# Performance work log

Hardware: AMD Instinct MI355X
Metric: run time of the kernel (lower is better)

## Reference

```python
import jax, jax.numpy as jnp
import numpy as np

N_NODES = 50000
N_EDGES = 1_600_000
N_REL = 8
D_IN = 128
D_OUT = 128


def _unique_edges(rng, n_nodes, n_rel, n_edges):
    # Torch module clamps the dense adjacency to 0/1, so duplicate
    # (rel, src, dst) triples collapse; generate unique edges so the
    # edge-list formulation matches exactly.
    m = 2 * n_edges
    src = rng.integers(0, n_nodes, m)
    dst = rng.integers(0, n_nodes, m)
    et = rng.integers(0, n_rel, m)
    key = (et.astype(np.int64) * n_nodes + src) * n_nodes + dst
    _, idx = np.unique(key, return_index=True)
    idx = np.sort(idx)[:n_edges]
    return src[idx], dst[idx], et[idx]


def setup_inputs() -> dict:
    key = jax.random.key(0)
    kx, kw, kr, kb = jax.random.split(key, 4)
    rng = np.random.default_rng(0)
    src, dst, et = _unique_edges(rng, N_NODES, N_REL, N_EDGES)
    bound = 1.0 / np.sqrt(D_OUT)
    return {
        "x": jax.random.normal(kx, (N_NODES, D_IN), dtype=jnp.float32),
        "edge_index": jnp.asarray(np.stack([src, dst]), dtype=jnp.int64),
        "edge_type": jnp.asarray(et, dtype=jnp.int64),
        "weight": jax.random.uniform(kw, (N_REL, D_OUT, D_IN), minval=-bound, maxval=bound, dtype=jnp.float32),
        "root": jax.random.uniform(kr, (D_OUT, D_IN), minval=-bound, maxval=bound, dtype=jnp.float32),
        "bias": jax.random.uniform(kb, (D_OUT,), minval=-bound, maxval=bound, dtype=jnp.float32),
    }


def reference(x, edge_index, edge_type, weight, root, bias):
    # Math identical to: adj[l, src, dst] = 1; adj row-normalized (mean);
    # out = sum_r norm_adj_r @ x @ W_r^T + x @ root^T + bias.
    n_rel, d_out, d_in = weight.shape
    n_nodes = x.shape[0]
    src = edge_index[0]
    dst = edge_index[1]
    seg = (edge_type * n_nodes + src).astype(jnp.int32)  # segment per (rel, node)
    num_seg = n_rel * n_nodes
    # sum of neighbor features per (relation, node): [R*N, d_in]
    agg = jax.ops.segment_sum(x[dst], seg, num_segments=num_seg)
    deg = jax.ops.segment_sum(jnp.ones((src.shape[0],), dtype=x.dtype), seg, num_segments=num_seg)
    norm = jnp.where(deg > 0, 1.0 / deg, 0.0)[:, None]  # mean aggr, nan_to_num(0)
    agg = (agg * norm).reshape(n_rel, n_nodes, d_in)
    out = jnp.einsum('rnd,rod->no', agg, weight)
    out = out + x @ root.T + bias[None]
    return out
```

## Files before the change

kernel.cpp:

```cpp
#include <hip/hip_runtime.h>


#define D 128
#define SCAN_CHUNK 2048
#define SEG_BITS 9
#define SEGS_PER_BUCKET 512
#define NBLK 128
#define NDEG 32

typedef __attribute__((ext_vector_type(8))) short short8;
typedef __attribute__((ext_vector_type(4))) float v4f;
typedef __attribute__((ext_vector_type(2))) float f32x2;
typedef __attribute__((ext_vector_type(4))) unsigned uint4v;

#define GLOAD_LDS16(gptr, lptr) \
    __builtin_amdgcn_global_load_lds((const __attribute__((address_space(1))) void*)(gptr), \
                                     (__attribute__((address_space(3))) void*)(lptr), 16, 0, 0)

__device__ __forceinline__ unsigned short f2b(float f) {
    union { float f; unsigned u; } v; v.f = f;
    unsigned r = v.u + 0x7fffu + ((v.u >> 16) & 1u);
    return (unsigned short)(r >> 16);
}
__device__ __forceinline__ float blo(unsigned u) {
    union { unsigned u; float f; } v; v.u = u << 16; return v.f;
}
__device__ __forceinline__ float bhi(unsigned u) {
    union { unsigned u; float f; } v; v.u = u & 0xffff0000u; return v.f;
}

__global__ void cvt_bf16_all(const float* __restrict__ x, long long nx,
                             const float* __restrict__ w, long long nw,
                             const float* __restrict__ root, long long nr,
                             unsigned short* __restrict__ xB,
                             unsigned short* __restrict__ xRow,
                             unsigned short* __restrict__ wB, int nN) {
    long long i = ((long long)blockIdx.x * blockDim.x + threadIdx.x) * 4;
    if (i < nx) {
        float4 v = *(const float4*)(x + i);
        uint2 p;
        p.x = (unsigned)f2b(v.x) | ((unsigned)f2b(v.y) << 16);
        p.y = (unsigned)f2b(v.z) | ((unsigned)f2b(v.w) << 16);
        long long n = i >> 7;
        int d = (int)(i & 127);
        size_t o = (size_t)(d >> 5) * (size_t)nN * 32 + (size_t)n * 32 + (d & 31);
        *(uint2*)(xB + o) = p;
        *(uint2*)(xRow + i) = p;
        return;
    }
    const float* src;
    unsigned short* dst;
    long long j;
    if (i < nx + nw) { src = w; dst = wB; j = i - nx; }
    else if (i < nx + nw + nr) { src = root; dst = wB + nw; j = i - nx - nw; }
    else return;
    float4 v = *(const float4*)(src + j);
    uint2 p;
    p.x = (unsigned)f2b(v.x) | ((unsigned)f2b(v.y) << 16);
    p.y = (unsigned)f2b(v.z) | ((unsigned)f2b(v.w) << 16);
    *(uint2*)(dst + j) = p;
}

__global__ __launch_bounds__(256)
void histA(const int* __restrict__ ei, const int* __restrict__ et,
           int* __restrict__ blockHist, int nE, int nN, int B, int epb) {
    __shared__ int lh[1024];
    const int tid = threadIdx.x;
    for (int b = tid; b < B; b += 256) lh[b] = 0;
    __syncthreads();
    const int base = blockIdx.x * epb;
    const int lim = min(base + epb, nE);
    for (int e = base + tid; e < lim; e += 256) {
        int seg = et[e] * nN + ei[e];
        atomicAdd(&lh[seg >> SEG_BITS], 1);
    }
    __syncthreads();
    for (int b = tid; b < B; b += 256)
        blockHist[b * NBLK + blockIdx.x] = lh[b];
}

__global__ __launch_bounds__(256)
void scan1(const int* __restrict__ in, int* __restrict__ excl,
           int* __restrict__ blockSums, int n) {
    __shared__ int t[256];
    const int tid = threadIdx.x;
    const int base = blockIdx.x * SCAN_CHUNK + tid * 8;
    int v[8];
    int tot = 0;
#pragma unroll
    for (int i = 0; i < 8; i++) {
        v[i] = (base + i < n) ? in[base + i] : 0;
        tot += v[i];
    }
    t[tid] = tot;
    __syncthreads();
    for (int off = 1; off < 256; off <<= 1) {
        int add = (tid >= off) ? t[tid - off] : 0;
        __syncthreads();
        t[tid] += add;
        __syncthreads();
    }
    int run = t[tid] - tot;
#pragma unroll
    for (int i = 0; i < 8; i++) {
        if (base + i < n) excl[base + i] = run;
        run += v[i];
    }
    if (tid == 255) blockSums[blockIdx.x] = t[255];
}

__global__ __launch_bounds__(256)
void scan2(int* __restrict__ blockSums, int nb) {
    __shared__ int t[256];
    const int tid = threadIdx.x;
    int v = (tid < nb) ? blockSums[tid] : 0;
    t[tid] = v;
    __syncthreads();
    for (int off = 1; off < 256; off <<= 1) {
        int add = (tid >= off) ? t[tid - off] : 0;
        __syncthreads();
        t[tid] += add;
        __syncthreads();
    }
    if (tid < nb) blockSums[tid] = t[tid] - v;
}

__global__ __launch_bounds__(256)
void scatterA(const int* __restrict__ ei, const int* __restrict__ et,
              const int* __restrict__ scanned, const int* __restrict__ blockSums,
              unsigned* __restrict__ bucketEdges,
              int nE, int nN, int B, int epb) {
    __shared__ int cur[1024];
    const int tid = threadIdx.x;
    for (int b = tid; b < B; b += 256) {
        int idx = b * NBLK + blockIdx.x;
        cur[b] = scanned[idx] + blockSums[idx >> 11];
    }
    __syncthreads();
    const int base = blockIdx.x * epb;
    const int lim = min(base + epb, nE);
    for (int e = base + tid; e < lim; e += 256) {
        int seg = et[e] * nN + ei[e];
        int bkt = seg >> SEG_BITS;
        unsigned pk = ((unsigned)(seg & (SEGS_PER_BUCKET - 1)) << 16) | (unsigned)ei[nE + e];
        int pos = atomicAdd(&cur[bkt], 1);
        bucketEdges[pos] = pk;
    }
}

__global__ __launch_bounds__(256)
void segOff(const unsigned* __restrict__ bucketEdges, const int* __restrict__ scanned,
            const int* __restrict__ blockSums,
            int* __restrict__ off, unsigned short* __restrict__ sortedDst,
            int* __restrict__ perm, int nE, int numSeg, int B) {
    __shared__ int lh[SEGS_PER_BUCKET];
    __shared__ int sc[256];
    __shared__ int lcur[SEGS_PER_BUCKET];
    __shared__ int dcnt[256];
    __shared__ int dbase[256];
    const int tid = threadIdx.x;
    const int b = blockIdx.x;
    const int i0 = b * NBLK;
    const int eBase = scanned[i0] + blockSums[i0 >> 11];
    int eEnd = nE;
    if (b + 1 < B) {
        const int i1 = (b + 1) * NBLK;
        eEnd = scanned[i1] + blockSums[i1 >> 11];
    }
    const int segBase = b * SEGS_PER_BUCKET;
    const int segLim = min(SEGS_PER_BUCKET, numSeg - segBase);

    lh[2 * tid] = 0; lh[2 * tid + 1] = 0;
    dcnt[tid] = 0;
    __syncthreads();
    for (int i = eBase + tid; i < eEnd; i += 256)
        atomicAdd(&lh[bucketEdges[i] >> 16], 1);
    __syncthreads();
    const int li0 = 2 * tid, li1 = 2 * tid + 1;
    const int sub = li0 >> 6;
    int a0 = lh[li0], a1 = lh[li1];
    int b0 = min(a0, NDEG - 1), b1 = min(a1, NDEG - 1), r0 = 0, r1 = 0;
    if (li0 < segLim) r0 = atomicAdd(&dcnt[sub * NDEG + b0], 1);
    if (li1 < segLim) r1 = atomicAdd(&dcnt[sub * NDEG + b1], 1);
    sc[tid] = a0 + a1;
    __syncthreads();
    for (int o = 1; o < 256; o <<= 1) {
        int add = (tid >= o) ? sc[tid - o] : 0;
        __syncthreads();
        sc[tid] += add;
        __syncthreads();
    }
    int pairBase = sc[tid] - (a0 + a1);
    int g0 = eBase + pairBase;
    int g1 = g0 + a0;
    lcur[li0] = g0;
    lcur[li1] = g1;
    if (li0 < segLim) off[segBase + li0] = g0;
    if (li1 < segLim) off[segBase + li1] = g1;
    if (b == B - 1 && tid == 0) off[numSeg] = nE;
    if (tid < 8) {
        int run = 0;
#pragma unroll
        for (int k = 0; k < NDEG; k++) { dbase[tid * NDEG + k] = run; run += dcnt[tid * NDEG + k]; }
    }
    __syncthreads();
    if (li0 < segLim) perm[segBase + sub * 64 + dbase[sub * NDEG + b0] + r0] = segBase + li0;
    if (li1 < segLim) perm[segBase + sub * 64 + dbase[sub * NDEG + b1] + r1] = segBase + li1;
    for (int i = eBase + tid; i < eEnd; i += 256) {
        unsigned u = bucketEdges[i];
        int pos = atomicAdd(&lcur[u >> 16], 1);
        sortedDst[pos] = (unsigned short)(u & 0xFFFFu);
    }
}

__global__ __launch_bounds__(256)
void rgcn_gather(const unsigned short* __restrict__ xB,
                 const unsigned short* __restrict__ sortedDst,
                 const int* __restrict__ off, const int* __restrict__ perm,
                 unsigned short* __restrict__ Abuf, int nN, int numSeg,
                 size_t SL, unsigned long long M) {
    const int tid = threadIdx.x;
    const int lane = tid & 63;
    const int idx4 = lane & 3;
    const int grp = lane >> 2;
    const int wv = tid >> 6;
    const int gsi = blockIdx.x * 64 + wv * 16 + grp;
    const int sl = blockIdx.y;
    const bool valid = (gsi < numSeg);
    const int seg = valid ? perm[gsi] : 0;

    const int start = off[seg];
    int cnt = valid ? (off[seg + 1] - start) : 0;

    int mx = cnt;
    mx = max(mx, __shfl_xor(mx, 4));
    mx = max(mx, __shfl_xor(mx, 8));
    mx = max(mx, __shfl_xor(mx, 16));
    mx = max(mx, __shfl_xor(mx, 32));

    f32x2 acc2[4];
#pragma unroll
    for (int i = 0; i < 4; i++) acc2[i] = (f32x2){0.f, 0.f};

    const unsigned short* xSlab = xB + (size_t)sl * nN * 32 + idx4 * 8;

    for (int b = 0; b < mx; b += 4) {
        int myDst = (b + idx4 < cnt) ? (int)sortedDst[start + b + idx4] : 0;
        uint4v v[4];
#pragma unroll
        for (int j = 0; j < 4; j++) {
            int dst = __shfl(myDst, grp * 4 + j);
            bool act = (b + j < cnt);
            v[j] = act ? *(const uint4v*)(xSlab + ((size_t)dst << 5))
                       : (uint4v){0u, 0u, 0u, 0u};
        }
#pragma unroll
        for (int j = 0; j < 4; j++) {
            f32x2 t0 = (f32x2){blo(v[j].x), bhi(v[j].x)};
            f32x2 t1 = (f32x2){blo(v[j].y), bhi(v[j].y)};
            f32x2 t2 = (f32x2){blo(v[j].z), bhi(v[j].z)};
            f32x2 t3 = (f32x2){blo(v[j].w), bhi(v[j].w)};
            asm("v_pk_add_f32 %0, %0, %1" : "+v"(acc2[0]) : "v"(t0));
            asm("v_pk_add_f32 %0, %0, %1" : "+v"(acc2[1]) : "v"(t1));
            asm("v_pk_add_f32 %0, %0, %1" : "+v"(acc2[2]) : "v"(t2));
            asm("v_pk_add_f32 %0, %0, %1" : "+v"(acc2[3]) : "v"(t3));
        }
    }

    if (valid) {
        const int r = (int)(((unsigned long long)seg * M) >> 48);
        const int n = seg - r * nN;
        float s = cnt > 0 ? 1.0f / (float)cnt : 0.f;
        uint4v pkt;
        pkt.x = (unsigned)f2b(acc2[0].x * s) | ((unsigned)f2b(acc2[0].y * s) << 16);
        pkt.y = (unsigned)f2b(acc2[1].x * s) | ((unsigned)f2b(acc2[1].y * s) << 16);
        pkt.z = (unsigned)f2b(acc2[2].x * s) | ((unsigned)f2b(acc2[2].y * s) << 16);
        pkt.w = (unsigned)f2b(acc2[3].x * s) | ((unsigned)f2b(acc2[3].y * s) << 16);
        __builtin_nontemporal_store(pkt,
            (uint4v*)(Abuf + (size_t)r * SL + (size_t)n * D + sl * 32 + idx4 * 8));
    }
}

__global__ __launch_bounds__(256)
void rgcn_gemm_mfma(const unsigned short* __restrict__ A,
                    const unsigned short* __restrict__ wB,
                    const float* __restrict__ bias,
                    float* __restrict__ out, int nN, int nRel, size_t SL) {
    __shared__ __align__(16) unsigned short As[2][64 * 64];
    __shared__ __align__(16) unsigned short Bs[2][128 * 64];
    const int tid = threadIdx.x;
    const int wave = tid >> 6;
    const int lane = tid & 63;
    const int wm = wave & 1;
    const int wn = wave >> 1;
    const int m16 = lane & 15;
    const int q = lane >> 4;
    const int row0 = blockIdx.x * 64;

    v4f acc[2][4];
#pragma unroll
    for (int i = 0; i < 2; i++)
#pragma unroll
        for (int j = 0; j < 4; j++) acc[i][j] = (v4f){0.f, 0.f, 0.f, 0.f};

    const int sw = m16 & 7;
    int aoff[2][2], boff[4][2];
#pragma unroll
    for (int mt = 0; mt < 2; mt++) {
        int row = wm * 32 + mt * 16 + m16;
#pragma unroll
        for (int kb = 0; kb < 2; kb++)
            aoff[mt][kb] = row * 64 + (((kb * 4 + q) ^ sw) * 8);
    }
#pragma unroll
    for (int nt = 0; nt < 4; nt++) {
        int o = wn * 64 + nt * 16 + m16;
#pragma unroll
        for (int kb = 0; kb < 2; kb++)
            boff[nt][kb] = o * 64 + (((kb * 4 + q) ^ sw) * 8);
    }

    const int l8 = lane >> 3;
    const int gd = (lane & 7) ^ l8;
    const size_t aBase = (size_t)(row0 + wave * 16 + l8) * D + gd * 8;
    const size_t bBase = (size_t)(wave * 32 + l8) * D + gd * 8;

    const int nT = 2 * (nRel + 1);

#define STAGE(buf, t) do { \
        const int s_ = (t) >> 1, h_ = (t) & 1; \
        const unsigned short* ga_ = A + (size_t)s_ * SL + h_ * 64 + aBase; \
        const unsigned short* gb_ = wB + (size_t)s_ * (D * D) + h_ * 64 + bBase; \
        GLOAD_LDS16(ga_,        &As[buf][(wave * 2 + 0) * 512]); \
        GLOAD_LDS16(ga_ + 1024, &As[buf][(wave * 2 + 1) * 512]); \
        GLOAD_LDS16(gb_,        &Bs[buf][(wave * 4 + 0) * 512]); \
        GLOAD_LDS16(gb_ + 1024, &Bs[buf][(wave * 4 + 1) * 512]); \
        GLOAD_LDS16(gb_ + 2048, &Bs[buf][(wave * 4 + 2) * 512]); \
        GLOAD_LDS16(gb_ + 3072, &Bs[buf][(wave * 4 + 3) * 512]); \
    } while (0)

    STAGE(0, 0);
    __syncthreads();
    int cur = 0;
    for (int t = 0; t < nT; ++t) {
        if (t + 1 < nT) STAGE(cur ^ 1, t + 1);
        const unsigned short* Ab = As[cur];
        const unsigned short* Bb = Bs[cur];
        short8 a[2][2], b[4][2];
#pragma unroll
        for (int kb = 0; kb < 2; kb++) {
#pragma unroll
            for (int mt = 0; mt < 2; mt++)
                a[mt][kb] = *(const short8*)&Ab[aoff[mt][kb]];
#pragma unroll
            for (int nt = 0; nt < 4; nt++)
                b[nt][kb] = *(const short8*)&Bb[boff[nt][kb]];
        }
#pragma unroll
        for (int kb = 0; kb < 2; kb++)
#pragma unroll
            for (int mt = 0; mt < 2; mt++)
#pragma unroll
                for (int nt = 0; nt < 4; nt++)
                    acc[mt][nt] = __builtin_amdgcn_mfma_f32_16x16x32_bf16(
                        a[mt][kb], b[nt][kb], acc[mt][nt], 0, 0, 0);
        __syncthreads();
        cur ^= 1;
    }
#undef STAGE

#pragma unroll
    for (int mt = 0; mt < 2; mt++) {
#pragma unroll
        for (int nt = 0; nt < 4; nt++) {
            int col = wn * 64 + nt * 16 + m16;
            float bi = bias[col];
#pragma unroll
            for (int reg = 0; reg < 4; reg++) {
                int rrow = row0 + wm * 32 + mt * 16 + q * 4 + reg;
                if (rrow < nN)
                    out[(size_t)rrow * D + col] = acc[mt][nt][reg] + bi;
            }
        }
    }
}

extern "C" void kernel_launch(void* const* d_in, const int* in_sizes, int n_in,
                              void* d_out, int out_size, void* d_ws, size_t ws_size,
                              hipStream_t stream) {
    const float* x    = (const float*)d_in[0];
    const int*   ei   = (const int*)d_in[1];
    const int*   et   = (const int*)d_in[2];
    const float* w    = (const float*)d_in[3];
    const float* root = (const float*)d_in[4];
    const float* bias = (const float*)d_in[5];
    float* out = (float*)d_out;

    const int nN   = in_sizes[0] / D;
    const int nE   = in_sizes[2];
    const int nRel = in_sizes[3] / (D * D);
    const int numSeg = nRel * nN;
    const int B = (numSeg + SEGS_PER_BUCKET - 1) >> SEG_BITS;
    const int nBH = B * NBLK;
    const int epb = (nE + NBLK - 1) / NBLK;
    const int nNalloc = (nN + 63) & ~63;
    const size_t SL = (size_t)nNalloc * D;
    const unsigned long long M = ((1ULL << 48) + nN - 1) / nN;

    char* p = (char*)d_ws;
    unsigned* bucketEdges   = (unsigned*)p;        p += (size_t)nE * sizeof(unsigned);
    unsigned short* sortedDst = (unsigned short*)p; p += (size_t)nE * sizeof(unsigned short);
    p = (char*)(((uintptr_t)p + 255) & ~(uintptr_t)255);
    int* off       = (int*)p;  p += (size_t)(numSeg + 1) * sizeof(int);
    int* blockHist = (int*)p;  p += (size_t)nBH * sizeof(int);
    int* scanned   = (int*)p;  p += (size_t)nBH * sizeof(int);
    int* blockSums = (int*)p;  p += 256 * sizeof(int);
    p = (char*)(((uintptr_t)p + 255) & ~(uintptr_t)255);
    int* perm      = (int*)p;  p += (size_t)numSeg * sizeof(int);
    p = (char*)(((uintptr_t)p + 255) & ~(uintptr_t)255);
    unsigned short* xB   = (unsigned short*)p;  p += (size_t)nN * D * sizeof(unsigned short);
    unsigned short* wBc  = (unsigned short*)p;  p += (size_t)(nRel + 1) * D * D * sizeof(unsigned short);
    p = (char*)(((uintptr_t)p + 255) & ~(uintptr_t)255);
    unsigned short* Abuf = (unsigned short*)p;
    unsigned short* xRow = Abuf + (size_t)nRel * SL;

    const int nScanBlocks = (nBH + SCAN_CHUNK - 1) / SCAN_CHUNK;

    histA<<<NBLK, 256, 0, stream>>>(ei, et, blockHist, nE, nN, B, epb);
    scan1<<<nScanBlocks, 256, 0, stream>>>(blockHist, scanned, blockSums, nBH);
    scan2<<<1, 256, 0, stream>>>(blockSums, nScanBlocks);
    scatterA<<<NBLK, 256, 0, stream>>>(ei, et, scanned, blockSums, bucketEdges, nE, nN, B, epb);
    segOff<<<B, 256, 0, stream>>>(bucketEdges, scanned, blockSums, off, sortedDst, perm,
                                  nE, numSeg, B);

    long long nx = (long long)nN * D;
    long long nw = (long long)nRel * D * D;
    long long nr = (long long)D * D;
    long long ncvt = (nx + nw + nr) / 4;
    cvt_bf16_all<<<(int)((ncvt + 255) / 256), 256, 0, stream>>>(x, nx, w, nw, root, nr,
                                                                xB, xRow, wBc, nN);

    dim3 gg((numSeg + 63) / 64, 4);
    rgcn_gather<<<gg, 256, 0, stream>>>(xB, sortedDst, off, perm, Abuf, nN, numSeg, SL, M);

    rgcn_gemm_mfma<<<(nN + 63) / 64, 256, 0, stream>>>(Abuf, wBc, bias, out, nN, nRel, SL);
}
```

Before: 269.1 us.

## Pack segment records, precompute per-group max degree, gather two segments per lane group

segOff now writes one packed record per degree-sorted slot (start, count, segment id), replacing the separate perm and off arrays. It also writes a precomputed max degree for each group of 16 slots. The gather kernel reads a single int4 per segment instead of chasing perm then off, and uses the precomputed wave-uniform max instead of a shuffle reduction. Each lane group now handles two segments to raise memory-level parallelism, and the bf16 pack uses the hardware cvt_pk instruction. The cost is more registers and twice as many CTAs' worth of work per block, which may lower occupancy.

```diff
diff --git a/kernel.cpp b/kernel.cpp
--- a/kernel.cpp
+++ b/kernel.cpp
@@ -151,13 +151,14 @@
 __global__ __launch_bounds__(256)
 void segOff(const unsigned* __restrict__ bucketEdges, const int* __restrict__ scanned,
             const int* __restrict__ blockSums,
-            int* __restrict__ off, unsigned short* __restrict__ sortedDst,
-            int* __restrict__ perm, int nE, int numSeg, int B) {
+            int4* __restrict__ permRec, unsigned short* __restrict__ sortedDst,
+            int* __restrict__ permMax, int nE, int numSeg, int B) {
     __shared__ int lh[SEGS_PER_BUCKET];
     __shared__ int sc[256];
     __shared__ int lcur[SEGS_PER_BUCKET];
     __shared__ int dcnt[256];
     __shared__ int dbase[256];
+    __shared__ int smax[32];
     const int tid = threadIdx.x;
     const int b = blockIdx.x;
     const int i0 = b * NBLK;
@@ -172,6 +173,7 @@
 
     lh[2 * tid] = 0; lh[2 * tid + 1] = 0;
     dcnt[tid] = 0;
+    if (tid < 32) smax[tid] = 0;
     __syncthreads();
     for (int i = eBase + tid; i < eEnd; i += 256)
         atomicAdd(&lh[bucketEdges[i] >> 16], 1);
@@ -195,28 +197,36 @@
     int g1 = g0 + a0;
     lcur[li0] = g0;
     lcur[li1] = g1;
-    if (li0 < segLim) off[segBase + li0] = g0;
-    if (li1 < segLim) off[segBase + li1] = g1;
-    if (b == B - 1 && tid == 0) off[numSeg] = nE;
     if (tid < 8) {
         int run = 0;
 #pragma unroll
         for (int k = 0; k < NDEG; k++) { dbase[tid * NDEG + k] = run; run += dcnt[tid * NDEG + k]; }
     }
     __syncthreads();
-    if (li0 < segLim) perm[segBase + sub * 64 + dbase[sub * NDEG + b0] + r0] = segBase + li0;
-    if (li1 < segLim) perm[segBase + sub * 64 + dbase[sub * NDEG + b1] + r1] = segBase + li1;
+    if (li0 < segLim) {
+        int rk = dbase[sub * NDEG + b0] + r0;
+        permRec[segBase + sub * 64 + rk] = make_int4(g0, a0, segBase + li0, 0);
+        atomicMax(&smax[(sub << 2) + (rk >> 4)], a0);
+    }
+    if (li1 < segLim) {
+        int rk = dbase[sub * NDEG + b1] + r1;
+        permRec[segBase + sub * 64 + rk] = make_int4(g1, a1, segBase + li1, 0);
+        atomicMax(&smax[(sub << 2) + (rk >> 4)], a1);
+    }
     for (int i = eBase + tid; i < eEnd; i += 256) {
         unsigned u = bucketEdges[i];
         int pos = atomicAdd(&lcur[u >> 16], 1);
         sortedDst[pos] = (unsigned short)(u & 0xFFFFu);
     }
+    __syncthreads();
+    if (tid < 32) permMax[b * 32 + tid] = smax[tid];
 }
 
 __global__ __launch_bounds__(256)
 void rgcn_gather(const unsigned short* __restrict__ xB,
                  const unsigned short* __restrict__ sortedDst,
-                 const int* __restrict__ off, const int* __restrict__ perm,
+                 const int4* __restrict__ permRec,
+                 const int* __restrict__ permMax,
                  unsigned short* __restrict__ Abuf, int nN, int numSeg,
                  size_t SL, unsigned long long M) {
     const int tid = threadIdx.x;
@@ -224,58 +234,113 @@
     const int idx4 = lane & 3;
     const int grp = lane >> 2;
     const int wv = tid >> 6;
-    const int gsi = blockIdx.x * 64 + wv * 16 + grp;
+    const int gsi0 = blockIdx.x * 128 + wv * 32 + grp;
+    const int gsi1 = gsi0 + 16;
     const int sl = blockIdx.y;
-    const bool valid = (gsi < numSeg);
-    const int seg = valid ? perm[gsi] : 0;
-
-    const int start = off[seg];
-    int cnt = valid ? (off[seg + 1] - start) : 0;
-
-    int mx = cnt;
-    mx = max(mx, __shfl_xor(mx, 4));
-    mx = max(mx, __shfl_xor(mx, 8));
-    mx = max(mx, __shfl_xor(mx, 16));
-    mx = max(mx, __shfl_xor(mx, 32));
-
-    f32x2 acc2[4];
-#pragma unroll
-    for (int i = 0; i < 4; i++) acc2[i] = (f32x2){0.f, 0.f};
+    const bool v0 = (gsi0 < numSeg);
+    const bool v1 = (gsi1 < numSeg);
+
+    int4 rc0 = v0 ? permRec[gsi0] : make_int4(0, 0, 0, 0);
+    int4 rc1 = v1 ? permRec[gsi1] : make_int4(0, 0, 0, 0);
+    int mx0 = v0 ? permMax[gsi0 >> 4] : 0;
+    int mx1 = v1 ? permMax[gsi1 >> 4] : 0;
+    mx0 = __builtin_amdgcn_readfirstlane(mx0);
+    mx1 = __builtin_amdgcn_readfirstlane(mx1);
+
+    const int start0 = rc0.x, cnt0 = v0 ? rc0.y : 0, seg0 = rc0.z;
+    const int start1 = rc1.x, cnt1 = v1 ? rc1.y : 0, seg1 = rc1.z;
+
+    f32x2 a0[4], a1[4];
+#pragma unroll
+    for (int i = 0; i < 4; i++) { a0[i] = (f32x2){0.f, 0.f}; a1[i] = (f32x2){0.f, 0.f}; }
 
     const unsigned short* xSlab = xB + (size_t)sl * nN * 32 + idx4 * 8;
 
-    for (int b = 0; b < mx; b += 4) {
-        int myDst = (b + idx4 < cnt) ? (int)sortedDst[start + b + idx4] : 0;
-        uint4v v[4];
-#pragma unroll
-        for (int j = 0; j < 4; j++) {
-            int dst = __shfl(myDst, grp * 4 + j);
-            bool act = (b + j < cnt);
-            v[j] = act ? *(const uint4v*)(xSlab + ((size_t)dst << 5))
-                       : (uint4v){0u, 0u, 0u, 0u};
+    const int mxm = max(mx0, mx1);
+    for (int b = 0; b < mxm; b += 4) {
+        uint4v w0[4], w1[4];
+        int myD0 = 0, myD1 = 0;
+        if (b < mx0) myD0 = (b + idx4 < cnt0) ? (int)sortedDst[start0 + b + idx4] : 0;
+        if (b < mx1) myD1 = (b + idx4 < cnt1) ? (int)sortedDst[start1 + b + idx4] : 0;
+        if (b < mx0) {
+#pragma unroll
+            for (int j = 0; j < 4; j++) {
+                int dst = __shfl(myD0, grp * 4 + j);
+                bool act = (b + j < cnt0);
+                w0[j] = act ? *(const uint4v*)(xSlab + ((size_t)dst << 5))
+                            : (uint4v){0u, 0u, 0u, 0u};
+            }
         }
-#pragma unroll
-        for (int j = 0; j < 4; j++) {
-            f32x2 t0 = (f32x2){blo(v[j].x), bhi(v[j].x)};
-            f32x2 t1 = (f32x2){blo(v[j].y), bhi(v[j].y)};
-            f32x2 t2 = (f32x2){blo(v[j].z), bhi(v[j].z)};
-            f32x2 t3 = (f32x2){blo(v[j].w), bhi(v[j].w)};
-            asm("v_pk_add_f32 %0, %0, %1" : "+v"(acc2[0]) : "v"(t0));
-            asm("v_pk_add_f32 %0, %0, %1" : "+v"(acc2[1]) : "v"(t1));
-            asm("v_pk_add_f32 %0, %0, %1" : "+v"(acc2[2]) : "v"(t2));
-            asm("v_pk_add_f32 %0, %0, %1" : "+v"(acc2[3]) : "v"(t3));
+        if (b < mx1) {
+#pragma unroll
+            for (int j = 0; j < 4; j++) {
+                int dst = __shfl(myD1, grp * 4 + j);
+                bool act = (b + j < cnt1);
+                w1[j] = act ? *(const uint4v*)(xSlab + ((size_t)dst << 5))
+                            : (uint4v){0u, 0u, 0u, 0u};
+            }
         }
-    }
-
-    if (valid) {
-        const int r = (int)(((unsigned long long)seg * M) >> 48);
-        const int n = seg - r * nN;
-        float s = cnt > 0 ? 1.0f / (float)cnt : 0.f;
-        uint4v pkt;
-        pkt.x = (unsigned)f2b(acc2[0].x * s) | ((unsigned)f2b(acc2[0].y * s) << 16);
-        pkt.y = (unsigned)f2b(acc2[1].x * s) | ((unsigned)f2b(acc2[1].y * s) << 16);
-        pkt.z = (unsigned)f2b(acc2[2].x * s) | ((unsigned)f2b(acc2[2].y * s) << 16);
-        pkt.w = (unsigned)f2b(acc2[3].x * s) | ((unsigned)f2b(acc2[3].y * s) << 16);
+        if (b < mx0) {
+#pragma unroll
+            for (int j = 0; j < 4; j++) {
+                f32x2 t0 = (f32x2){blo(w0[j].x), bhi(w0[j].x)};
+                f32x2 t1 = (f32x2){blo(w0[j].y), bhi(w0[j].y)};
+                f32x2 t2 = (f32x2){blo(w0[j].z), bhi(w0[j].z)};
+                f32x2 t3 = (f32x2){blo(w0[j].w), bhi(w0[j].w)};
+                asm("v_pk_add_f32 %0, %0, %1" : "+v"(a0[0]) : "v"(t0));
+                asm("v_pk_add_f32 %0, %0, %1" : "+v"(a0[1]) : "v"(t1));
+                asm("v_pk_add_f32 %0, %0, %1" : "+v"(a0[2]) : "v"(t2));
+                asm("v_pk_add_f32 %0, %0, %1" : "+v"(a0[3]) : "v"(t3));
+            }
+        }
+        if (b < mx1) {
+#pragma unroll
+            for (int j = 0; j < 4; j++) {
+                f32x2 t0 = (f32x2){blo(w1[j].x), bhi(w1[j].x)};
+                f32x2 t1 = (f32x2){blo(w1[j].y), bhi(w1[j].y)};
+                f32x2 t2 = (f32x2){blo(w1[j].z), bhi(w1[j].z)};
+                f32x2 t3 = (f32x2){blo(w1[j].w), bhi(w1[j].w)};
+                asm("v_pk_add_f32 %0, %0, %1" : "+v"(a1[0]) : "v"(t0));
+                asm("v_pk_add_f32 %0, %0, %1" : "+v"(a1[1]) : "v"(t1));
+                asm("v_pk_add_f32 %0, %0, %1" : "+v"(a1[2]) : "v"(t2));
+                asm("v_pk_add_f32 %0, %0, %1" : "+v"(a1[3]) : "v"(t3));
+            }
+        }
+    }
+
+    if (v0) {
+        float s = cnt0 > 0 ? 1.0f / (float)cnt0 : 0.f;
+        const int r = (int)(((unsigned long long)seg0 * M) >> 48);
+        const int n = seg0 - r * nN;
+        unsigned p0, p1, p2, p3;
+        float e0, e1;
+        e0 = a0[0].x * s; e1 = a0[0].y * s;
+        asm("v_cvt_pk_bf16_f32 %0, %1, %2" : "=v"(p0) : "v"(e0), "v"(e1));
+        e0 = a0[1].x * s; e1 = a0[1].y * s;
+        asm("v_cvt_pk_bf16_f32 %0, %1, %2" : "=v"(p1) : "v"(e0), "v"(e1));
+        e0 = a0[2].x * s; e1 = a0[2].y * s;
+        asm("v_cvt_pk_bf16_f32 %0, %1, %2" : "=v"(p2) : "v"(e0), "v"(e1));
+        e0 = a0[3].x * s; e1 = a0[3].y * s;
+        asm("v_cvt_pk_bf16_f32 %0, %1, %2" : "=v"(p3) : "v"(e0), "v"(e1));
+        uint4v pkt = (uint4v){p0, p1, p2, p3};
+        __builtin_nontemporal_store(pkt,
+            (uint4v*)(Abuf + (size_t)r * SL + (size_t)n * D + sl * 32 + idx4 * 8));
+    }
+    if (v1) {
+        float s = cnt1 > 0 ? 1.0f / (float)cnt1 : 0.f;
+        const int r = (int)(((unsigned long long)seg1 * M) >> 48);
+        const int n = seg1 - r * nN;
+        unsigned p0, p1, p2, p3;
+        float e0, e1;
+        e0 = a1[0].x * s; e1 = a1[0].y * s;
+        asm("v_cvt_pk_bf16_f32 %0, %1, %2" : "=v"(p0) : "v"(e0), "v"(e1));
+        e0 = a1[1].x * s; e1 = a1[1].y * s;
+        asm("v_cvt_pk_bf16_f32 %0, %1, %2" : "=v"(p1) : "v"(e0), "v"(e1));
+        e0 = a1[2].x * s; e1 = a1[2].y * s;
+        asm("v_cvt_pk_bf16_f32 %0, %1, %2" : "=v"(p2) : "v"(e0), "v"(e1));
+        e0 = a1[3].x * s; e1 = a1[3].y * s;
+        asm("v_cvt_pk_bf16_f32 %0, %1, %2" : "=v"(p3) : "v"(e0), "v"(e1));
+        uint4v pkt = (uint4v){p0, p1, p2, p3};
         __builtin_nontemporal_store(pkt,
             (uint4v*)(Abuf + (size_t)r * SL + (size_t)n * D + sl * 32 + idx4 * 8));
     }
@@ -411,12 +476,12 @@
     unsigned* bucketEdges   = (unsigned*)p;        p += (size_t)nE * sizeof(unsigned);
     unsigned short* sortedDst = (unsigned short*)p; p += (size_t)nE * sizeof(unsigned short);
     p = (char*)(((uintptr_t)p + 255) & ~(uintptr_t)255);
-    int* off       = (int*)p;  p += (size_t)(numSeg + 1) * sizeof(int);
     int* blockHist = (int*)p;  p += (size_t)nBH * sizeof(int);
     int* scanned   = (int*)p;  p += (size_t)nBH * sizeof(int);
     int* blockSums = (int*)p;  p += 256 * sizeof(int);
     p = (char*)(((uintptr_t)p + 255) & ~(uintptr_t)255);
-    int* perm      = (int*)p;  p += (size_t)numSeg * sizeof(int);
+    int4* permRec  = (int4*)p; p += (size_t)numSeg * sizeof(int4);
+    int* permMax   = (int*)p;  p += (size_t)B * 32 * sizeof(int);
     p = (char*)(((uintptr_t)p + 255) & ~(uintptr_t)255);
     unsigned short* xB   = (unsigned short*)p;  p += (size_t)nN * D * sizeof(unsigned short);
     unsigned short* wBc  = (unsigned short*)p;  p += (size_t)(nRel + 1) * D * D * sizeof(unsigned short);
@@ -430,7 +495,7 @@
     scan1<<<nScanBlocks, 256, 0, stream>>>(blockHist, scanned, blockSums, nBH);
     scan2<<<1, 256, 0, stream>>>(blockSums, nScanBlocks);
     scatterA<<<NBLK, 256, 0, stream>>>(ei, et, scanned, blockSums, bucketEdges, nE, nN, B, epb);
-    segOff<<<B, 256, 0, stream>>>(bucketEdges, scanned, blockSums, off, sortedDst, perm,
+    segOff<<<B, 256, 0, stream>>>(bucketEdges, scanned, blockSums, permRec, sortedDst, permMax,
                                   nE, numSeg, B);
 
     long long nx = (long long)nN * D;
@@ -440,8 +505,8 @@
     cvt_bf16_all<<<(int)((ncvt + 255) / 256), 256, 0, stream>>>(x, nx, w, nw, root, nr,
                                                                 xB, xRow, wBc, nN);
 
-    dim3 gg((numSeg + 63) / 64, 4);
-    rgcn_gather<<<gg, 256, 0, stream>>>(xB, sortedDst, off, perm, Abuf, nN, numSeg, SL, M);
+    dim3 gg((numSeg + 127) / 128, 4);
+    rgcn_gather<<<gg, 256, 0, stream>>>(xB, sortedDst, permRec, permMax, Abuf, nN, numSeg, SL, M);
 
     rgcn_gemm_mfma<<<(nN + 63) / 64, 256, 0, stream>>>(Abuf, wBc, bias, out, nN, nRel, SL);
 }
```

Measured after the change: 268.0 us. Within noise of the previous version (-0.4%).
